# Performance work log

Hardware: AMD Instinct MI355X
Metric: run time of the kernel (lower is better)

## Reference

```python
import jax, jax.numpy as jnp
import numpy as np

W_DIM, T_DIM = 300, 100
IN = W_DIM + T_DIM        # 400, also LSTM hidden size
H = IN                    # hiddenSize
BI = 2 * H                # 800, biLSTM output per step
MLP_IN = 2 * BI           # 1600
VOCAB, NTAGS = 50000, 50
SEQ = 320


def _lstm_dir(xs, w_ih, w_hh, b_ih, b_hh, h0, c0, reverse):
    # xs: [T, d_in]; PyTorch gate order i, f, g, o
    if reverse:
        xs = xs[::-1]
    def step(carry, x):
        h, c = carry
        g = x @ w_ih.T + h @ w_hh.T + b_ih + b_hh
        i, f, gc, o = jnp.split(g, 4)
        i, f, o = jax.nn.sigmoid(i), jax.nn.sigmoid(f), jax.nn.sigmoid(o)
        c = f * c + i * jnp.tanh(gc)
        h = o * jnp.tanh(c)
        return (h, c), h
    _, ys = jax.lax.scan(step, (h0, c0), xs)
    return ys[::-1] if reverse else ys


def _bilstm(x, params, h0, c0):
    # x: [T, IN]; h0/c0: [4, H] ordered (l0 fwd, l0 bwd, l1 fwd, l1 bwd)
    out = x
    for layer in range(2):
        p_f = params[layer][0]
        p_b = params[layer][1]
        yf = _lstm_dir(out, *p_f, h0[2 * layer],     c0[2 * layer],     False)
        yb = _lstm_dir(out, *p_b, h0[2 * layer + 1], c0[2 * layer + 1], True)
        out = jnp.concatenate([yf, yb], axis=-1)  # [T, 2H]
    return out


def setup_inputs() -> dict:
    key = jax.random.key(0)
    ks = iter(jax.random.split(key, 32))
    inp = {}
    inp['words'] = jax.random.randint(next(ks), (SEQ,), 0, VOCAB)
    inp['tags'] = jax.random.randint(next(ks), (SEQ,), 0, NTAGS)
    inp['arcs'] = jax.random.randint(next(ks), (SEQ + 1,), 0, SEQ + 1)
    inp['word_emb'] = jax.random.normal(next(ks), (VOCAB, W_DIM), jnp.float32) * 0.1
    inp['tag_emb'] = jax.random.normal(next(ks), (NTAGS, T_DIM), jnp.float32) * 0.1
    inp['h0'] = jax.random.normal(next(ks), (4, H), jnp.float32)
    inp['c0'] = jax.random.normal(next(ks), (4, H), jnp.float32)
    s = 1.0 / np.sqrt(H)
    for layer, d_in in ((0, IN), (1, BI)):
        for suf in ('', 'r'):
            inp[f'w_ih_l{layer}{suf}'] = jax.random.uniform(next(ks), (4 * H, d_in), jnp.float32, -s, s)
            inp[f'w_hh_l{layer}{suf}'] = jax.random.uniform(next(ks), (4 * H, H), jnp.float32, -s, s)
            inp[f'b_ih_l{layer}{suf}'] = jax.random.uniform(next(ks), (4 * H,), jnp.float32, -s, s)
            inp[f'b_hh_l{layer}{suf}'] = jax.random.uniform(next(ks), (4 * H,), jnp.float32, -s, s)
    inp['mlp_w1'] = jax.random.normal(next(ks), (MLP_IN, MLP_IN), jnp.float32) * 0.02
    inp['mlp_b1'] = jnp.zeros((MLP_IN,), jnp.float32)
    inp['mlp_w2'] = jax.random.normal(next(ks), (1, MLP_IN), jnp.float32) * 0.02
    inp['mlp_b2'] = jnp.zeros((1,), jnp.float32)
    return inp


def reference(words, tags, arcs, word_emb, tag_emb, h0, c0,
              w_ih_l0, w_hh_l0, b_ih_l0, b_hh_l0,
              w_ih_l0r, w_hh_l0r, b_ih_l0r, b_hh_l0r,
              w_ih_l1, w_hh_l1, b_ih_l1, b_hh_l1,
              w_ih_l1r, w_hh_l1r, b_ih_l1r, b_hh_l1r,
              mlp_w1, mlp_b1, mlp_w2, mlp_b2):
    n = words.shape[0]
    x = jnp.concatenate([word_emb[words], tag_emb[tags]], axis=1)  # [n, IN]
    params = (((w_ih_l0, w_hh_l0, b_ih_l0, b_hh_l0), (w_ih_l0r, w_hh_l0r, b_ih_l0r, b_hh_l0r)),
              ((w_ih_l1, w_hh_l1, b_ih_l1, b_hh_l1), (w_ih_l1r, w_hh_l1r, b_ih_l1r, b_hh_l1r)))
    hv = _bilstm(x, params, h0, c0)  # [n, BI]
    # pairwise MLP: concat(h_head, h_dep) @ W1.T == h_head @ W1a.T + h_dep @ W1b.T
    w1a, w1b = mlp_w1[:, :BI], mlp_w1[:, BI:]
    a = hv @ w1a.T  # [n, MLP_IN], head part
    b = hv @ w1b.T  # [n, MLP_IN], dep part
    hid = jax.nn.relu(a[:, None, :] + b[None, :, :] + mlp_b1)  # [n, n, MLP_IN]
    scores = jnp.einsum('ndk,ok->nd', hid, mlp_w2)[..., 0] if mlp_w2.shape[0] != 1 else (hid @ mlp_w2[0] + mlp_b2[0])  # [n, n]
    offdiag = 1.0 - jnp.eye(n, dtype=scores.dtype)
    score_tensor = jnp.zeros((n + 1, n + 1), scores.dtype)
    score_tensor = score_tensor.at[0, 0].set(1.0)
    score_tensor = score_tensor.at[1:, 1:].set(scores * offdiag)
    return score_tensor
```

## Files before the change

kernel.cpp:

```cpp
#include <hip/hip_runtime.h>
#include <hip/hip_bf16.h>
#include <hip/hip_fp16.h>

#define SEQ   320
#define GATES 1600
#define NCOL  3200
#define GDW   16
#define RPW   25

typedef _Float16 half2v __attribute__((ext_vector_type(2)));
typedef _Float16 f16x8  __attribute__((ext_vector_type(8)));
typedef float    f32x4  __attribute__((ext_vector_type(4)));
union H2U { unsigned u; half2v h; __half2 hh; };

__global__ __launch_bounds__(256) void prep_kernel(
    const int* __restrict__ words, const int* __restrict__ tags,
    const float* __restrict__ wemb, const float* __restrict__ temb,
    _Float16* __restrict__ Ah0,
    const float* __restrict__ bihl0,  const float* __restrict__ bhhl0,
    const float* __restrict__ bihl0r, const float* __restrict__ bhhl0r,
    const float* __restrict__ bihl1,  const float* __restrict__ bhhl1,
    const float* __restrict__ bihl1r, const float* __restrict__ bhhl1r,
    const float* __restrict__ mlpb1,
    float* __restrict__ bL0, float* __restrict__ bL1, float* __restrict__ bAB,
    const float* __restrict__ wih0, const float* __restrict__ wih0r,
    _Float16* __restrict__ BhA)
{
    const int b = blockIdx.x, t = threadIdx.x;
    if (b < 520) {
        int i = b * 256 + t;
        if (i >= SEQ * 416) return;
        int tt = i / 416, c = i % 416;
        float v = 0.f;
        if (c < 300)      v = wemb[(size_t)words[tt] * 300 + c];
        else if (c < 400) v = temb[(size_t)tags[tt] * 100 + (c - 300)];
        Ah0[i] = (_Float16)v;
    } else if (b < 533) {
        int g = (b - 520) * 256 + t;
        if (g >= NCOL) return;
        if (g < GATES) {
            bL0[g] = bihl0[g] + bhhl0[g];
            bL1[g] = bihl1[g] + bhhl1[g];
            bAB[g] = mlpb1[g];
        } else {
            int q = g - GATES;
            bL0[g] = bihl0r[q] + bhhl0r[q];
            bL1[g] = bihl1r[q] + bhhl1r[q];
            bAB[g] = 0.f;
        }
    } else {
        int i = (b - 533) * 256 + t;
        if (i >= NCOL * 416) return;
        int n = i / 416, k = i % 416;
        float v = 0.f;
        if (k < 400)
            v = (n < GATES) ? wih0[(size_t)n * 400 + k]
                            : wih0r[(size_t)(n - GATES) * 400 + k];
        BhA[i] = (_Float16)v;
    }
}

__global__ __launch_bounds__(256) void cvt2_kernel(
    const float* __restrict__ wih1, const float* __restrict__ wih1r,
    _Float16* __restrict__ BhB,
    const float* __restrict__ mlpw1, _Float16* __restrict__ BhA)
{
    const int b = blockIdx.x, t = threadIdx.x;
    if (b < 10000) {
        int i = b * 256 + t;
        if (i >= NCOL * 800) return;
        int n = i / 800, k = i % 800;
        BhB[i] = (_Float16)((n < GATES) ? wih1[(size_t)n * 800 + k]
                                        : wih1r[(size_t)(n - GATES) * 800 + k]);
    } else {
        int i = (b - 10000) * 256 + t;
        if (i >= NCOL * 800) return;
        int n = i / 800, k = i % 800;
        BhA[i] = (_Float16)((n < GATES) ? mlpw1[(size_t)n * 1600 + k]
                                        : mlpw1[(size_t)(n - GATES) * 1600 + 800 + k]);
    }
}

__global__ __launch_bounds__(256) void gemm_f16(
    const _Float16* __restrict__ A, int Kp,
    const _Float16* __restrict__ B,
    const float* __restrict__ bias, float* __restrict__ C)
{
    const int tid  = threadIdx.x;
    const int w    = tid >> 6, lane = tid & 63;
    const int quad = lane >> 4, l16 = lane & 15;
    const int mb   = blockIdx.y * 32 + (w & 1) * 16;
    const int n0   = blockIdx.x * 64 + (w >> 1) * 32;
    const _Float16* Arow = A + (size_t)(mb + l16) * Kp + quad * 8;
    const _Float16* B0r  = B + (size_t)(n0 + l16) * Kp + quad * 8;
    const _Float16* B1r  = B0r + (size_t)16 * Kp;
    f32x4 acc0 = {0.f, 0.f, 0.f, 0.f}, acc1 = {0.f, 0.f, 0.f, 0.f};
#pragma unroll 4
    for (int k0 = 0; k0 < Kp; k0 += 32) {
        f16x8 a  = *(const f16x8*)(Arow + k0);
        f16x8 b0 = *(const f16x8*)(B0r + k0);
        f16x8 b1 = *(const f16x8*)(B1r + k0);
        acc0 = __builtin_amdgcn_mfma_f32_16x16x32_f16(a, b0, acc0, 0, 0, 0);
        acc1 = __builtin_amdgcn_mfma_f32_16x16x32_f16(a, b1, acc1, 0, 0, 0);
    }
    const int mr = mb + quad * 4;
    float bn0 = bias[n0 + l16], bn1 = bias[n0 + 16 + l16];
#pragma unroll
    for (int r = 0; r < 4; ++r) {
        C[(size_t)(mr + r) * NCOL + n0 + l16]      = acc0[r] + bn0;
        C[(size_t)(mr + r) * NCOL + n0 + 16 + l16] = acc1[r] + bn1;
    }
}

__global__ __launch_bounds__(1024, 4) void lstm_layer(
    const float* __restrict__ gates,
    const float* __restrict__ whh_f, const float* __restrict__ whh_b,
    const float* __restrict__ h0f, const float* __restrict__ h0b,
    const float* __restrict__ c0f, const float* __restrict__ c0b,
    unsigned* __restrict__ ex,
    _Float16* __restrict__ ah)
{
    __shared__ unsigned h_pk[200];
    __shared__ float part[16][28];
    unsigned short* hs = (unsigned short*)h_pk;
    const int tid = threadIdx.x;
    const int dir = blockIdx.x >> 4;
    const int wg  = blockIdx.x & 15;
    const int j0  = wg * RPW;
    const float* whh = dir ? whh_b : whh_f;
    const float* h0d = dir ? h0b : h0f;
    const float* c0d = dir ? c0b : c0f;

    const int w    = tid >> 6;
    const int lane = tid & 63;
    const int g    = w & 3;
    const int kq   = w >> 2;
    const int half = lane & 1;
    const int r    = lane >> 1;
    const int jrow = j0 + (r < RPW ? r : RPW - 1);

    unsigned wr[26];
    {
        const float2* wp = (const float2*)(whh + (size_t)(g * 400 + jrow) * 400 +
                                           kq * 100 + 48 * half);
#pragma unroll
        for (int i = 0; i < 26; ++i) {
            H2U cv; float2 f = wp[i];
            cv.hh = __floats2half2_rn(f.x, f.y);
            wr[i] = (half == 0 && i >= 24) ? 0u : cv.u;
        }
    }

    const int pp = tid / 13;
    const int pd = tid - pp * 13;
    float c_prev = (tid < RPW) ? c0d[j0 + tid] : 0.f;

    for (int s = 0; s < 320; ++s) {
        const int row = dir ? (319 - s) : s;

        float gv0 = 0.f, gv1 = 0.f, gv2 = 0.f, gv3 = 0.f;
        if (tid < RPW) {
            const float* gx = gates + (size_t)row * NCOL + dir * GATES + j0 + tid;
            gv0 = gx[0]; gv1 = gx[400]; gv2 = gx[800]; gv3 = gx[1200];
        }

        if (s == 0) {
            if (tid < 100) {
                float4 f = ((const float4*)h0d)[tid];
                H2U a, b;
                a.hh = __floats2half2_rn(f.x, f.y);
                b.hh = __floats2half2_rn(f.z, f.w);
                ((uint2*)h_pk)[tid] = make_uint2(a.u, b.u);
            }
        } else if (tid < 208 && pp != wg) {
            const int rp = dir ? (row + 1) : (row - 1);
            const unsigned* src = ex + (((size_t)dir * GDW + pp) * SEQ + rp) * 16 + pd;
            unsigned v;
            for (;;) {
                v = __hip_atomic_load(src, __ATOMIC_RELAXED, __HIP_MEMORY_SCOPE_AGENT);
                if ((v & 0xFFFFu) != 0xFFFFu &&
                    (pd == 12 || (v >> 16) != 0xFFFFu)) break;
            }
            const int hb = pp * RPW + pd * 2;
            hs[hb] = (unsigned short)(v & 0xFFFFu);
            if (pd < 12) hs[hb + 1] = (unsigned short)(v >> 16);
        }
        __syncthreads();

        {
            const uint2* hp2 = (const uint2*)h_pk + kq * 25 + 12 * half;
            float acc = 0.f;
#pragma unroll
            for (int i = 0; i < 13; ++i) {
                uint2 hv2 = hp2[i];
                H2U w0, w1, x0, x1;
                w0.u = wr[2 * i]; w1.u = wr[2 * i + 1];
                x0.u = hv2.x;     x1.u = hv2.y;
                acc = __builtin_amdgcn_fdot2(w0.h, x0.h, acc, false);
                acc = __builtin_amdgcn_fdot2(w1.h, x1.h, acc, false);
            }
            acc += __shfl_xor(acc, 1, 64);
            if (half == 0 && r < RPW) part[w][r] = acc;
        }
        __syncthreads();

        float hv = 0.f;
        if (tid < RPW) {
            float gi = gv0 + ((part[0][tid] + part[4][tid]) + (part[8][tid]  + part[12][tid]));
            float gf = gv1 + ((part[1][tid] + part[5][tid]) + (part[9][tid]  + part[13][tid]));
            float gg = gv2 + ((part[2][tid] + part[6][tid]) + (part[10][tid] + part[14][tid]));
            float go = gv3 + ((part[3][tid] + part[7][tid]) + (part[11][tid] + part[15][tid]));
            float iv = 1.f / (1.f + __expf(-gi));
            float fv = 1.f / (1.f + __expf(-gf));
            float ov = 1.f / (1.f + __expf(-go));
            float tg = 1.f - 2.f / (1.f + __expf(2.f * gg));
            c_prev = fv * c_prev + iv * tg;
            float tc = 1.f - 2.f / (1.f + __expf(2.f * c_prev));
            hv = ov * tc;
        }
        if (w == 0) {
            int i0 = 2 * lane     < 63 ? 2 * lane     : 63;
            int i1 = 2 * lane + 1 < 63 ? 2 * lane + 1 : 63;
            float xlo = __shfl(hv, i0, 64);
            float xhi = __shfl(hv, i1, 64);
            if (lane < 13) {
                H2U pk;
                pk.hh = __floats2half2_rn(xlo, (2 * lane + 1 < RPW) ? xhi : 0.f);
                __hip_atomic_store(ex + (((size_t)dir * GDW + wg) * SEQ + row) * 16 + lane,
                                   pk.u, __ATOMIC_RELAXED, __HIP_MEMORY_SCOPE_AGENT);
            }
            if (tid < RPW) {
                ah[(size_t)row * 800 + dir * 400 + j0 + tid] = (_Float16)hv;
                H2U o; o.hh = __floats2half2_rn(hv, 0.f);
                hs[RPW * wg + tid] = (unsigned short)(o.u & 0xFFFFu);
            }
        }
    }
}

__global__ __launch_bounds__(256) void scores_kernel(
    const float* __restrict__ ab, const float* __restrict__ w2,
    const float* __restrict__ b2, float* __restrict__ out)
{
    if (blockIdx.y == 20) {
        int i = blockIdx.x * 256 + threadIdx.y * 16 + threadIdx.x;
        if (blockIdx.x < 2 && i < 321) {
            out[i]               = (i == 0) ? 1.f : 0.f;
            out[(size_t)i * 321] = (i == 0) ? 1.f : 0.f;
        }
        return;
    }
    __shared__ float a_s[16 * 132];
    __shared__ float b_s[16 * 132];
    __shared__ float w_s[128];
    const int tx = threadIdx.x, ty = threadIdx.y;
    const int tid = ty * 16 + tx;
    const int n0 = blockIdx.y * 16, d0 = blockIdx.x * 16;
    float acc = 0.f;
    for (int kc = 0; kc < 1600; kc += 128) {
        for (int i = tid; i < 16 * 128; i += 256) {
            int r = i >> 7, c = i & 127;
            a_s[r * 132 + c] = ab[(size_t)(n0 + r) * NCOL + kc + c];
            b_s[r * 132 + c] = ab[(size_t)(d0 + r) * NCOL + 1600 + kc + c];
        }
        if (tid < 128) w_s[tid] = w2[kc + tid];
        __syncthreads();
#pragma unroll
        for (int k = 0; k < 128; k += 4) {
            float4 av = *(const float4*)&a_s[ty * 132 + k];
            float4 bv = *(const float4*)&b_s[tx * 132 + k];
            float4 wv = *(const float4*)&w_s[k];
            acc += fmaxf(av.x + bv.x, 0.f) * wv.x;
            acc += fmaxf(av.y + bv.y, 0.f) * wv.y;
            acc += fmaxf(av.z + bv.z, 0.f) * wv.z;
            acc += fmaxf(av.w + bv.w, 0.f) * wv.w;
        }
        __syncthreads();
    }
    int n = n0 + ty, d = d0 + tx;
    out[(size_t)(n + 1) * 321 + (d + 1)] = (n == d) ? 0.f : (acc + b2[0]);
}

extern "C" void kernel_launch(void* const* d_in, const int* in_sizes, int n_in,
                              void* d_out, int out_size, void* d_ws, size_t ws_size,
                              hipStream_t stream)
{
    const int*   words    = (const int*)d_in[0];
    const int*   tags     = (const int*)d_in[1];
    const float* wemb     = (const float*)d_in[3];
    const float* temb     = (const float*)d_in[4];
    const float* h0       = (const float*)d_in[5];
    const float* c0       = (const float*)d_in[6];
    const float* w_ih_l0  = (const float*)d_in[7];
    const float* w_hh_l0  = (const float*)d_in[8];
    const float* b_ih_l0  = (const float*)d_in[9];
    const float* b_hh_l0  = (const float*)d_in[10];
    const float* w_ih_l0r = (const float*)d_in[11];
    const float* w_hh_l0r = (const float*)d_in[12];
    const float* b_ih_l0r = (const float*)d_in[13];
    const float* b_hh_l0r = (const float*)d_in[14];
    const float* w_ih_l1  = (const float*)d_in[15];
    const float* w_hh_l1  = (const float*)d_in[16];
    const float* b_ih_l1  = (const float*)d_in[17];
    const float* b_hh_l1  = (const float*)d_in[18];
    const float* w_ih_l1r = (const float*)d_in[19];
    const float* w_hh_l1r = (const float*)d_in[20];
    const float* b_ih_l1r = (const float*)d_in[21];
    const float* b_hh_l1r = (const float*)d_in[22];
    const float* mlp_w1   = (const float*)d_in[23];
    const float* mlp_b1   = (const float*)d_in[24];
    const float* mlp_w2   = (const float*)d_in[25];
    const float* mlp_b2   = (const float*)d_in[26];
    float* out = (float*)d_out;

    float* ws      = (float*)d_ws;
    float*    gates  = ws;
    float*    biasL0 = ws + 1024000;
    float*    biasL1 = ws + 1027200;
    float*    biasAB = ws + 1030400;
    unsigned* ex     = (unsigned*)(ws + 1033600);
    _Float16* Ah0    = (_Float16*)(ws + 1361280);
    _Float16* Ah1    = (_Float16*)(ws + 1427840);
    _Float16* Ah2    = (_Float16*)(ws + 1555840);
    _Float16* BhA    = (_Float16*)(ws + 1683840);
    _Float16* BhB    = (_Float16*)(ws + 2963840);
    unsigned* ex0 = ex, *ex1 = ex + 163840;

    hipMemsetAsync(ex, 0xFF, 327680u * 4, stream);

    prep_kernel<<<5733, 256, 0, stream>>>(
        words, tags, wemb, temb, Ah0,
        b_ih_l0, b_hh_l0, b_ih_l0r, b_hh_l0r,
        b_ih_l1, b_hh_l1, b_ih_l1r, b_hh_l1r,
        mlp_b1, biasL0, biasL1, biasAB, w_ih_l0, w_ih_l0r, BhA);

    gemm_f16<<<dim3(50, 10), 256, 0, stream>>>(Ah0, 416, BhA, biasL0, gates);
    cvt2_kernel<<<20000, 256, 0, stream>>>(w_ih_l1, w_ih_l1r, BhB, mlp_w1, BhA);
    lstm_layer<<<2 * GDW, 1024, 0, stream>>>(gates, w_hh_l0, w_hh_l0r,
                                             h0, h0 + 400, c0, c0 + 400, ex0, Ah1);
    gemm_f16<<<dim3(50, 10), 256, 0, stream>>>(Ah1, 800, BhB, biasL1, gates);
    lstm_layer<<<2 * GDW, 1024, 0, stream>>>(gates, w_hh_l1, w_hh_l1r,
                                             h0 + 800, h0 + 1200, c0 + 800, c0 + 1200,
                                             ex1, Ah2);
    gemm_f16<<<dim3(50, 10), 256, 0, stream>>>(Ah2, 800, BhA, biasAB, gates);

    scores_kernel<<<dim3(20, 21), dim3(16, 16), 0, stream>>>(gates, mlp_w2, mlp_b2, out);
}
```

Measured before the change: 1.357 ms.

## Read hidden state directly from exchange buffer, dropping LDS staging barrier

```diff
diff --git a/kernel.cpp b/kernel.cpp
--- a/kernel.cpp
+++ b/kernel.cpp
@@ -7,6 +7,7 @@
 #define NCOL  3200
 #define GDW   16
 #define RPW   25
+#define EXL   (GDW * 2 * 322 * 16)
 
 typedef _Float16 half2v __attribute__((ext_vector_type(2)));
 typedef _Float16 f16x8  __attribute__((ext_vector_type(8)));
@@ -24,7 +25,10 @@
     const float* __restrict__ mlpb1,
     float* __restrict__ bL0, float* __restrict__ bL1, float* __restrict__ bAB,
     const float* __restrict__ wih0, const float* __restrict__ wih0r,
-    _Float16* __restrict__ BhA)
+    _Float16* __restrict__ BhA,
+    const float* __restrict__ wih1, const float* __restrict__ wih1r,
+    _Float16* __restrict__ BhB,
+    const float* __restrict__ h0, unsigned* __restrict__ ex)
 {
     const int b = blockIdx.x, t = threadIdx.x;
     if (b < 520) {
@@ -48,7 +52,7 @@
             bL1[g] = bihl1r[q] + bhhl1r[q];
             bAB[g] = 0.f;
         }
-    } else {
+    } else if (b < 5733) {
         int i = (b - 533) * 256 + t;
         if (i >= NCOL * 416) return;
         int n = i / 416, k = i % 416;
@@ -57,28 +61,36 @@
             v = (n < GATES) ? wih0[(size_t)n * 400 + k]
                             : wih0r[(size_t)(n - GATES) * 400 + k];
         BhA[i] = (_Float16)v;
-    }
-}
-
-__global__ __launch_bounds__(256) void cvt2_kernel(
-    const float* __restrict__ wih1, const float* __restrict__ wih1r,
-    _Float16* __restrict__ BhB,
-    const float* __restrict__ mlpw1, _Float16* __restrict__ BhA)
-{
-    const int b = blockIdx.x, t = threadIdx.x;
-    if (b < 10000) {
-        int i = b * 256 + t;
+    } else if (b < 15733) {
+        int i = (b - 5733) * 256 + t;
         if (i >= NCOL * 800) return;
         int n = i / 800, k = i % 800;
         BhB[i] = (_Float16)((n < GATES) ? wih1[(size_t)n * 800 + k]
                                         : wih1r[(size_t)(n - GATES) * 800 + k]);
     } else {
-        int i = (b - 10000) * 256 + t;
-        if (i >= NCOL * 800) return;
-        int n = i / 800, k = i % 800;
-        BhA[i] = (_Float16)((n < GATES) ? mlpw1[(size_t)n * 1600 + k]
-                                        : mlpw1[(size_t)(n - GATES) * 1600 + 800 + k]);
-    }
+        if (t >= 64) return;
+        int layer = t >> 5, dir = (t >> 4) & 1, p = t & 15;
+        const float* hsrc = h0 + (size_t)(layer * 2 + dir) * 400 + p * 25;
+        unsigned slot = dir ? 321u : 0u;
+        unsigned* line = ex + (size_t)layer * EXL +
+                         (((unsigned)dir * GDW + p) * 322 + slot) * 16;
+        for (int d = 0; d < 13; ++d) {
+            float lo = hsrc[2 * d];
+            float hi = (2 * d + 1 < RPW) ? hsrc[2 * d + 1] : 0.f;
+            H2U pk; pk.hh = __floats2half2_rn(lo, hi);
+            line[d] = pk.u;
+        }
+    }
+}
+
+__global__ __launch_bounds__(256) void cvtMLP_kernel(
+    const float* __restrict__ mlpw1, _Float16* __restrict__ BhA)
+{
+    int i = blockIdx.x * 256 + threadIdx.x;
+    if (i >= NCOL * 800) return;
+    int n = i / 800, k = i % 800;
+    BhA[i] = (_Float16)((n < GATES) ? mlpw1[(size_t)n * 1600 + k]
+                                    : mlpw1[(size_t)(n - GATES) * 1600 + 800 + k]);
 }
 
 __global__ __launch_bounds__(256) void gemm_f16(
@@ -115,20 +127,16 @@
 __global__ __launch_bounds__(1024, 4) void lstm_layer(
     const float* __restrict__ gates,
     const float* __restrict__ whh_f, const float* __restrict__ whh_b,
-    const float* __restrict__ h0f, const float* __restrict__ h0b,
     const float* __restrict__ c0f, const float* __restrict__ c0b,
     unsigned* __restrict__ ex,
     _Float16* __restrict__ ah)
 {
-    __shared__ unsigned h_pk[200];
-    __shared__ float part[16][28];
-    unsigned short* hs = (unsigned short*)h_pk;
+    __shared__ float part[2][16][28];
     const int tid = threadIdx.x;
     const int dir = blockIdx.x >> 4;
     const int wg  = blockIdx.x & 15;
     const int j0  = wg * RPW;
     const float* whh = dir ? whh_b : whh_f;
-    const float* h0d = dir ? h0b : h0f;
     const float* c0d = dir ? c0b : c0f;
 
     const int w    = tid >> 6;
@@ -137,26 +145,31 @@
     const int kq   = w >> 2;
     const int half = lane & 1;
     const int r    = lane >> 1;
+    const bool act = (lane < 2 * RPW);
     const int jrow = j0 + (r < RPW ? r : RPW - 1);
+    const int p0   = 4 * kq + 2 * half;
+    const unsigned* exd = ex + (size_t)dir * (GDW * 322 * 16);
+    const unsigned* LB0 = exd + (size_t)p0 * (322 * 16);
+    const unsigned* LB1 = exd + (size_t)(p0 + 1) * (322 * 16);
 
     unsigned wr[26];
-    {
-        const float2* wp = (const float2*)(whh + (size_t)(g * 400 + jrow) * 400 +
-                                           kq * 100 + 48 * half);
-#pragma unroll
-        for (int i = 0; i < 26; ++i) {
-            H2U cv; float2 f = wp[i];
-            cv.hh = __floats2half2_rn(f.x, f.y);
-            wr[i] = (half == 0 && i >= 24) ? 0u : cv.u;
-        }
-    }
-
-    const int pp = tid / 13;
-    const int pd = tid - pp * 13;
+#pragma unroll
+    for (int l = 0; l < 2; ++l) {
+        const float* wsrc = whh + (size_t)(g * 400 + jrow) * 400 + (p0 + l) * RPW;
+#pragma unroll
+        for (int d = 0; d < 13; ++d) {
+            float lo = wsrc[2 * d];
+            float hi = (d < 12) ? wsrc[2 * d + 1] : 0.f;
+            H2U pk; pk.hh = __floats2half2_rn(lo, hi);
+            wr[l * 13 + d] = pk.u;
+        }
+    }
+
     float c_prev = (tid < RPW) ? c0d[j0 + tid] : 0.f;
 
     for (int s = 0; s < 320; ++s) {
-        const int row = dir ? (319 - s) : s;
+        const int row  = dir ? (319 - s) : s;
+        const int slot = dir ? (row + 2) : row;
 
         float gv0 = 0.f, gv1 = 0.f, gv2 = 0.f, gv3 = 0.f;
         if (tid < RPW) {
@@ -164,52 +177,47 @@
             gv0 = gx[0]; gv1 = gx[400]; gv2 = gx[800]; gv3 = gx[1200];
         }
 
-        if (s == 0) {
-            if (tid < 100) {
-                float4 f = ((const float4*)h0d)[tid];
-                H2U a, b;
-                a.hh = __floats2half2_rn(f.x, f.y);
-                b.hh = __floats2half2_rn(f.z, f.w);
-                ((uint2*)h_pk)[tid] = make_uint2(a.u, b.u);
+        float acc = 0.f;
+        if (act) {
+            const unsigned* L0 = LB0 + slot * 16;
+            const unsigned* L1 = LB1 + slot * 16;
+            unsigned ha[13], hb[13];
+#pragma unroll
+            for (int i = 0; i < 13; ++i)
+                ha[i] = __hip_atomic_load(L0 + i, __ATOMIC_RELAXED, __HIP_MEMORY_SCOPE_AGENT);
+#pragma unroll
+            for (int i = 0; i < 13; ++i)
+                hb[i] = __hip_atomic_load(L1 + i, __ATOMIC_RELAXED, __HIP_MEMORY_SCOPE_AGENT);
+#pragma unroll
+            for (int i = 0; i < 13; ++i)
+                while (ha[i] == 0xFFFFFFFFu)
+                    ha[i] = __hip_atomic_load(L0 + i, __ATOMIC_RELAXED, __HIP_MEMORY_SCOPE_AGENT);
+#pragma unroll
+            for (int i = 0; i < 13; ++i) {
+                H2U wv, xv; wv.u = wr[i]; xv.u = ha[i];
+                acc = __builtin_amdgcn_fdot2(wv.h, xv.h, acc, false);
             }
-        } else if (tid < 208 && pp != wg) {
-            const int rp = dir ? (row + 1) : (row - 1);
-            const unsigned* src = ex + (((size_t)dir * GDW + pp) * SEQ + rp) * 16 + pd;
-            unsigned v;
-            for (;;) {
-                v = __hip_atomic_load(src, __ATOMIC_RELAXED, __HIP_MEMORY_SCOPE_AGENT);
-                if ((v & 0xFFFFu) != 0xFFFFu &&
-                    (pd == 12 || (v >> 16) != 0xFFFFu)) break;
+#pragma unroll
+            for (int i = 0; i < 13; ++i)
+                while (hb[i] == 0xFFFFFFFFu)
+                    hb[i] = __hip_atomic_load(L1 + i, __ATOMIC_RELAXED, __HIP_MEMORY_SCOPE_AGENT);
+#pragma unroll
+            for (int i = 0; i < 13; ++i) {
+                H2U wv, xv; wv.u = wr[13 + i]; xv.u = hb[i];
+                acc = __builtin_amdgcn_fdot2(wv.h, xv.h, acc, false);
             }
-            const int hb = pp * RPW + pd * 2;
-            hs[hb] = (unsigned short)(v & 0xFFFFu);
-            if (pd < 12) hs[hb + 1] = (unsigned short)(v >> 16);
-        }
-        __syncthreads();
-
-        {
-            const uint2* hp2 = (const uint2*)h_pk + kq * 25 + 12 * half;
-            float acc = 0.f;
-#pragma unroll
-            for (int i = 0; i < 13; ++i) {
-                uint2 hv2 = hp2[i];
-                H2U w0, w1, x0, x1;
-                w0.u = wr[2 * i]; w1.u = wr[2 * i + 1];
-                x0.u = hv2.x;     x1.u = hv2.y;
-                acc = __builtin_amdgcn_fdot2(w0.h, x0.h, acc, false);
-                acc = __builtin_amdgcn_fdot2(w1.h, x1.h, acc, false);
-            }
-            acc += __shfl_xor(acc, 1, 64);
-            if (half == 0 && r < RPW) part[w][r] = acc;
-        }
+        }
+        acc += __shfl_xor(acc, 1, 64);
+        if (act && half == 0) part[s & 1][w][r] = acc;
         __syncthreads();
 
         float hv = 0.f;
         if (tid < RPW) {
-            float gi = gv0 + ((part[0][tid] + part[4][tid]) + (part[8][tid]  + part[12][tid]));
-            float gf = gv1 + ((part[1][tid] + part[5][tid]) + (part[9][tid]  + part[13][tid]));
-            float gg = gv2 + ((part[2][tid] + part[6][tid]) + (part[10][tid] + part[14][tid]));
-            float go = gv3 + ((part[3][tid] + part[7][tid]) + (part[11][tid] + part[15][tid]));
+            const float (*pb)[28] = part[s & 1];
+            float gi = gv0 + ((pb[0][tid] + pb[4][tid]) + (pb[8][tid]  + pb[12][tid]));
+            float gf = gv1 + ((pb[1][tid] + pb[5][tid]) + (pb[9][tid]  + pb[13][tid]));
+            float gg = gv2 + ((pb[2][tid] + pb[6][tid]) + (pb[10][tid] + pb[14][tid]));
+            float go = gv3 + ((pb[3][tid] + pb[7][tid]) + (pb[11][tid] + pb[15][tid]));
             float iv = 1.f / (1.f + __expf(-gi));
             float fv = 1.f / (1.f + __expf(-gf));
             float ov = 1.f / (1.f + __expf(-go));
@@ -226,14 +234,11 @@
             if (lane < 13) {
                 H2U pk;
                 pk.hh = __floats2half2_rn(xlo, (2 * lane + 1 < RPW) ? xhi : 0.f);
-                __hip_atomic_store(ex + (((size_t)dir * GDW + wg) * SEQ + row) * 16 + lane,
-                                   pk.u, __ATOMIC_RELAXED, __HIP_MEMORY_SCOPE_AGENT);
+                unsigned* dst = (unsigned*)exd + ((size_t)wg * 322 + row + 1) * 16 + lane;
+                __hip_atomic_store(dst, pk.u, __ATOMIC_RELAXED, __HIP_MEMORY_SCOPE_AGENT);
             }
-            if (tid < RPW) {
+            if (tid < RPW)
                 ah[(size_t)row * 800 + dir * 400 + j0 + tid] = (_Float16)hv;
-                H2U o; o.hh = __floats2half2_rn(hv, 0.f);
-                hs[RPW * wg + tid] = (unsigned short)(o.u & 0xFFFFu);
-            }
         }
     }
 }
@@ -313,35 +318,35 @@
     const float* mlp_b2   = (const float*)d_in[26];
     float* out = (float*)d_out;
 
-    float* ws      = (float*)d_ws;
+    float* ws = (float*)d_ws;
     float*    gates  = ws;
     float*    biasL0 = ws + 1024000;
     float*    biasL1 = ws + 1027200;
     float*    biasAB = ws + 1030400;
     unsigned* ex     = (unsigned*)(ws + 1033600);
-    _Float16* Ah0    = (_Float16*)(ws + 1361280);
-    _Float16* Ah1    = (_Float16*)(ws + 1427840);
-    _Float16* Ah2    = (_Float16*)(ws + 1555840);
-    _Float16* BhA    = (_Float16*)(ws + 1683840);
-    _Float16* BhB    = (_Float16*)(ws + 2963840);
-    unsigned* ex0 = ex, *ex1 = ex + 163840;
-
-    hipMemsetAsync(ex, 0xFF, 327680u * 4, stream);
-
-    prep_kernel<<<5733, 256, 0, stream>>>(
+    _Float16* Ah0    = (_Float16*)(ws + 1363328);
+    _Float16* Ah1    = (_Float16*)(ws + 1429888);
+    _Float16* Ah2    = (_Float16*)(ws + 1557888);
+    _Float16* BhA    = (_Float16*)(ws + 1685888);
+    _Float16* BhB    = (_Float16*)(ws + 2965888);
+    unsigned* ex0 = ex, *ex1 = ex + EXL;
+
+    hipMemsetAsync(ex, 0xFF, (size_t)2 * EXL * 4, stream);
+
+    prep_kernel<<<15734, 256, 0, stream>>>(
         words, tags, wemb, temb, Ah0,
         b_ih_l0, b_hh_l0, b_ih_l0r, b_hh_l0r,
         b_ih_l1, b_hh_l1, b_ih_l1r, b_hh_l1r,
-        mlp_b1, biasL0, biasL1, biasAB, w_ih_l0, w_ih_l0r, BhA);
+        mlp_b1, biasL0, biasL1, biasAB,
+        w_ih_l0, w_ih_l0r, BhA, w_ih_l1, w_ih_l1r, BhB, h0, ex);
 
     gemm_f16<<<dim3(50, 10), 256, 0, stream>>>(Ah0, 416, BhA, biasL0, gates);
-    cvt2_kernel<<<20000, 256, 0, stream>>>(w_ih_l1, w_ih_l1r, BhB, mlp_w1, BhA);
+    cvtMLP_kernel<<<10000, 256, 0, stream>>>(mlp_w1, BhA);
     lstm_layer<<<2 * GDW, 1024, 0, stream>>>(gates, w_hh_l0, w_hh_l0r,
-                                             h0, h0 + 400, c0, c0 + 400, ex0, Ah1);
+                                             c0, c0 + 400, ex0, Ah1);
     gemm_f16<<<dim3(50, 10), 256, 0, stream>>>(Ah1, 800, BhB, biasL1, gates);
     lstm_layer<<<2 * GDW, 1024, 0, stream>>>(gates, w_hh_l1, w_hh_l1r,
-                                             h0 + 800, h0 + 1200, c0 + 800, c0 + 1200,
-                                             ex1, Ah2);
+                                             c0 + 800, c0 + 1200, ex1, Ah2);
     gemm_f16<<<dim3(50, 10), 256, 0, stream>>>(Ah2, 800, BhA, biasAB, gates);
 
     scores_kernel<<<dim3(20, 21), dim3(16, 16), 0, stream>>>(gates, mlp_w2, mlp_b2, out);
```

Result: slower. 4.310 ms (+217.7%).
